# Optimization experiments

Hardware: AMD Instinct MI355X
Metric: run time of the kernel (lower is better)

Reference implementation:

```python
import jax, jax.numpy as jnp
import numpy as np

N = 100000      # nodes
E = 1600000     # edges (avg degree 16)
F_DIM = 64      # input feature
H = 64          # hidden1
D1 = 64         # decoder1
P = 200000      # number of query pairs
EPS = 0.0       # GIN eps (train_eps=False)


def setup_inputs() -> dict:
    key = jax.random.key(0)
    ks = jax.random.split(key, 12)
    x = jax.random.normal(ks[0], (N, F_DIM), jnp.float32)
    edge_index = jax.random.randint(ks[1], (2, E), 0, N, dtype=jnp.int32)
    curvature = jax.random.normal(ks[2], (E,), jnp.float32)
    idx = jax.random.randint(ks[3], (2, P), 0, N, dtype=jnp.int32)
    s1 = 1.0 / np.sqrt(F_DIM)
    s2 = 1.0 / np.sqrt(H)
    s3 = 1.0 / np.sqrt(4 * H)
    s4 = 1.0 / np.sqrt(D1)
    w1 = jax.random.uniform(ks[4], (F_DIM, H), jnp.float32, -s1, s1)
    b1 = jax.random.uniform(ks[5], (H,), jnp.float32, -s1, s1)
    w2 = jax.random.uniform(ks[6], (H, H), jnp.float32, -s2, s2)
    b2 = jax.random.uniform(ks[7], (H,), jnp.float32, -s2, s2)
    dw1 = jax.random.uniform(ks[8], (4 * H, D1), jnp.float32, -s3, s3)
    db1 = jax.random.uniform(ks[9], (D1,), jnp.float32, -s3, s3)
    dw2 = jax.random.uniform(ks[10], (D1, 1), jnp.float32, -s4, s4)
    db2 = jax.random.uniform(ks[11], (1,), jnp.float32, -s4, s4)
    return {"x": x, "edge_index": edge_index, "curvature": curvature, "idx": idx,
            "w1": w1, "b1": b1, "w2": w2, "b2": b2,
            "dw1": dw1, "db1": db1, "dw2": dw2, "db2": db2}


def reference(x, edge_index, curvature, idx, w1, b1, w2, b2, dw1, db1, dw2, db2):
    # curvature path: abs + dropout (eval mode => identity), result unused by output
    _ = jnp.abs(curvature)
    src, dst = edge_index[0], edge_index[1]
    # GIN aggregation with self-loops of weight 1: sum_j x_j + x_i
    agg = jax.ops.segment_sum(x[src], dst, num_segments=N) + x  # [N, F]
    h = (1.0 + EPS) * x + agg
    # nn = Linear -> ReLU -> Linear
    h = jnp.maximum(h @ w1 + b1, 0.0) @ w2 + b2                 # [N, H]
    h = jnp.maximum(h, 0.0)                                     # outer ReLU
    e1 = h[idx[0]]                                              # [P, H]
    e2 = h[idx[1]]                                              # [P, H]
    feat = jnp.concatenate([e1 + e2, e1 * e2, e1, e2], axis=1)  # [P, 4H]
    log = jnp.maximum(feat @ dw1 + db1, 0.0) @ dw2 + db2        # [P, 1]
    return log
```

## Files before the change

kernel.cpp:

```cpp
#include <hip/hip_runtime.h>
#include <hip/hip_bf16.h>
#include <hip/hip_fp16.h>
#include <cstdint>

#define N_NODES 100000
#define N_EDGES 1600000
#define FDIM 64
#define NPAIRS 200000
#define NB 391
#define BCAP 4864
#define SSTR 5632
#define EPB 6250

typedef __attribute__((ext_vector_type(8))) _Float16 half8;
typedef __attribute__((ext_vector_type(4))) float floatx4;

__global__ void __launch_bounds__(256) k0_fused(const float4* __restrict__ x4,
        __half* __restrict__ xh, const int* __restrict__ dst,
        int* __restrict__ matrix, int* __restrict__ ovfCnt) {
    __shared__ int hist[NB];
    int blk = blockIdx.x, tid = threadIdx.x;
    int i = blk * 256 + tid;
    if (i == 0) ovfCnt[0] = 0;
    float4 v = x4[i];
    ushort4 o;
    o.x = __half_as_ushort(__float2half(v.x));
    o.y = __half_as_ushort(__float2half(v.y));
    o.z = __half_as_ushort(__float2half(v.z));
    o.w = __half_as_ushort(__float2half(v.w));
    ((ushort4*)xh)[i] = o;
    if (blk < 256) {
        for (int j = tid; j < NB; j += 256) hist[j] = 0;
        __syncthreads();
        int base = blk * EPB;
        for (int j = tid; j < EPB; j += 256)
            atomicAdd(&hist[dst[base + j] >> 8], 1);
        __syncthreads();
        for (int j = tid; j < NB; j += 256) matrix[blk * NB + j] = hist[j];
    }
}

__global__ void __launch_bounds__(256) p1b_scan(int* __restrict__ matrix,
                                                int* __restrict__ bucketCnt) {
    __shared__ int s[256];
    int b = blockIdx.x, t = threadIdx.x;
    int v = matrix[t * NB + b];
    s[t] = v;
    __syncthreads();
    for (int off = 1; off < 256; off <<= 1) {
        int u = (t >= off) ? s[t - off] : 0;
        __syncthreads();
        s[t] += u;
        __syncthreads();
    }
    matrix[t * NB + b] = s[t] - v;
    if (t == 255) bucketCnt[b] = s[255];
}

__global__ void __launch_bounds__(1024) p1c_scatter(const int* __restrict__ src,
        const int* __restrict__ dst, const int* __restrict__ matrix,
        int* __restrict__ bucketArr, int* __restrict__ ovfCnt,
        int2* __restrict__ ovfList) {
    __shared__ int cur[NB];
    int tid = threadIdx.x, blk = blockIdx.x;
    for (int i = tid; i < NB; i += 1024) cur[i] = matrix[blk * NB + i];
    __syncthreads();
    int base = blk * EPB;
    for (int i = tid; i < EPB; i += 1024) {
        int e = base + i;
        int s = src[e], d = dst[e];
        int b = d >> 8;
        int pos = atomicAdd(&cur[b], 1);
        if (pos < BCAP) {
            bucketArr[(size_t)b * SSTR + pos] = ((d & 255) << 17) | s;
        } else {
            int idx = atomicAdd(ovfCnt, 1);
            ovfList[idx] = make_int2(d, s);
        }
    }
}

__global__ void __launch_bounds__(256) p2_build(int* __restrict__ bucketArr,
        const int* __restrict__ bucketCnt, int* __restrict__ rowptr,
        int* __restrict__ deg) {
    __shared__ int ebuf[BCAP];
    __shared__ int hist[256], sc[256], cur[256];
    int b = blockIdx.x, t = threadIdx.x;
    int cnt = bucketCnt[b];
    if (cnt > BCAP) cnt = BCAP;
    int* arr = bucketArr + (size_t)b * SSTR;
    hist[t] = 0;
    __syncthreads();
    for (int i = t; i < cnt; i += 256) {
        int e = arr[i];
        ebuf[i] = e;
        atomicAdd(&hist[(e >> 17) & 255], 1);
    }
    __syncthreads();
    int h = hist[t];
    int pc = (h + 3) & ~3;
    sc[t] = pc;
    __syncthreads();
    for (int off = 1; off < 256; off <<= 1) {
        int u = (t >= off) ? sc[t - off] : 0;
        __syncthreads();
        sc[t] += u;
        __syncthreads();
    }
    int rbase = sc[t] - pc;
    cur[t] = rbase;
    int n = (b << 8) + t;
    if (n < N_NODES) {
        rowptr[n] = b * SSTR + rbase;
        deg[n] = h;
    }
    __syncthreads();
    for (int i = t; i < cnt; i += 256) {
        int e = ebuf[i];
        int dl = (e >> 17) & 255;
        int pos = atomicAdd(&cur[dl], 1);
        arr[pos] = e & 0x1FFFF;
    }
}

__device__ __forceinline__ void addrow(float4& acc, const __half* __restrict__ xh,
                                       int s, int fq) {
    float2 raw = *(const float2*)(xh + (size_t)s * 64 + fq * 4);
    __half2 a = *(__half2*)&raw.x;
    __half2 b = *(__half2*)&raw.y;
    float2 fa = __half22float2(a);
    float2 fb = __half22float2(b);
    acc.x += fa.x; acc.y += fa.y; acc.z += fb.x; acc.w += fb.y;
}

__global__ void __launch_bounds__(256) k2_agg(const __half* __restrict__ xh,
                       __half* __restrict__ h0h, const int* __restrict__ deg,
                       const int* __restrict__ rowptr, const int* __restrict__ csr,
                       const int* __restrict__ ovfCnt,
                       const int2* __restrict__ ovfList,
                       const float* __restrict__ x) {
    int gid = blockIdx.x * 256 + threadIdx.x;
    int n = gid >> 4, fq = gid & 15;
    int dc = deg[n];
    const int4* srow = (const int4*)(csr + rowptr[n]);
    float2 raw = *(const float2*)(xh + (size_t)n * 64 + fq * 4);
    __half2 sa = *(__half2*)&raw.x;
    __half2 sb = *(__half2*)&raw.y;
    float2 fa = __half22float2(sa);
    float2 fb = __half22float2(sb);
    float4 acc = {2.f * fa.x, 2.f * fa.y, 2.f * fb.x, 2.f * fb.y};
    int oc = ovfCnt[0];
    if (oc > 0) {
        for (int i = 0; i < oc; ++i) {
            int2 e = ovfList[i];
            if (e.x == n) {
                const float* xr = x + (size_t)e.y * 64 + fq * 4;
                acc.x += xr[0]; acc.y += xr[1]; acc.z += xr[2]; acc.w += xr[3];
            }
        }
    }
    for (int i = 0; i < dc; i += 16) {
        int4 s4 = srow[i >> 2];
        int4 s5, s6, s7;
        if (i + 4 < dc)  s5 = srow[(i >> 2) + 1];
        if (i + 8 < dc)  s6 = srow[(i >> 2) + 2];
        if (i + 12 < dc) s7 = srow[(i >> 2) + 3];
        addrow(acc, xh, s4.x, fq);
        if (i + 1 < dc)  addrow(acc, xh, s4.y, fq);
        if (i + 2 < dc)  addrow(acc, xh, s4.z, fq);
        if (i + 3 < dc)  addrow(acc, xh, s4.w, fq);
        if (i + 4 < dc)  addrow(acc, xh, s5.x, fq);
        if (i + 5 < dc)  addrow(acc, xh, s5.y, fq);
        if (i + 6 < dc)  addrow(acc, xh, s5.z, fq);
        if (i + 7 < dc)  addrow(acc, xh, s5.w, fq);
        if (i + 8 < dc)  addrow(acc, xh, s6.x, fq);
        if (i + 9 < dc)  addrow(acc, xh, s6.y, fq);
        if (i + 10 < dc) addrow(acc, xh, s6.z, fq);
        if (i + 11 < dc) addrow(acc, xh, s6.w, fq);
        if (i + 12 < dc) addrow(acc, xh, s7.x, fq);
        if (i + 13 < dc) addrow(acc, xh, s7.y, fq);
        if (i + 14 < dc) addrow(acc, xh, s7.z, fq);
        if (i + 15 < dc) addrow(acc, xh, s7.w, fq);
    }
    ushort4 st;
    st.x = __half_as_ushort(__float2half(acc.x));
    st.y = __half_as_ushort(__float2half(acc.y));
    st.z = __half_as_ushort(__float2half(acc.z));
    st.w = __half_as_ushort(__float2half(acc.w));
    ((ushort4*)h0h)[(size_t)n * 16 + fq] = st;
}

__global__ void __launch_bounds__(256) k3_mfma(const __half* __restrict__ h,
        __half* __restrict__ hh, const float* __restrict__ w1,
        const float* __restrict__ b1, const float* __restrict__ w2,
        const float* __restrict__ b2) {
    __shared__ half8 WF1[512], WF2[512];
    __shared__ float Tbuf[4 * 16 * 68];
    int tid = threadIdx.x;
    for (int f = tid; f < 512; f += 256) {
        int lane = f & 63, st = f >> 6;
        int t = st & 3, kh = st >> 2;
        int q = lane >> 4, nl = lane & 15;
        int n = t * 16 + nl;
        int K0 = kh * 32 + q * 8;
        half8 hv1, hv2;
#pragma unroll
        for (int j = 0; j < 8; ++j) {
            hv1[j] = (_Float16)w1[(K0 + j) * 64 + n];
            hv2[j] = (_Float16)w2[(K0 + j) * 64 + n];
        }
        WF1[f] = hv1;
        WF2[f] = hv2;
    }
    __syncthreads();
    int lane = tid & 63;
    int q = lane >> 4, p = lane & 15;
    int wtid0 = blockIdx.x * 4 + (tid >> 6);
    int wtid = wtid0 < 6249 ? wtid0 : 6249;
    int n0 = wtid * 16;
    float b1t[4], b2t[4];
#pragma unroll
    for (int t = 0; t < 4; ++t) {
        b1t[t] = b1[t * 16 + p];
        b2t[t] = b2[t * 16 + p];
    }
    const half8* hrow = (const half8*)(h + (size_t)(n0 + p) * 64);
    half8 A0 = hrow[q], A1 = hrow[4 + q];
    floatx4 acc[4];
#pragma unroll
    for (int t = 0; t < 4; ++t) acc[t] = (floatx4){0.f, 0.f, 0.f, 0.f};
#pragma unroll
    for (int t = 0; t < 4; ++t) {
        acc[t] = __builtin_amdgcn_mfma_f32_16x16x32_f16(A0, WF1[t * 64 + lane],
                                                        acc[t], 0, 0, 0);
        acc[t] = __builtin_amdgcn_mfma_f32_16x16x32_f16(A1, WF1[(4 + t) * 64 + lane],
                                                        acc[t], 0, 0, 0);
    }
    float* T = Tbuf + (tid >> 6) * (16 * 68);
#pragma unroll
    for (int t = 0; t < 4; ++t) {
#pragma unroll
        for (int r = 0; r < 4; ++r)
            T[(q * 4 + r) * 68 + t * 16 + p] = fmaxf(acc[t][r] + b1t[t], 0.f);
    }
    const float* Tp = T + p * 68;
    float4 u0 = *(const float4*)(Tp + q * 8);
    float4 u1 = *(const float4*)(Tp + q * 8 + 4);
    float4 u2 = *(const float4*)(Tp + 32 + q * 8);
    float4 u3 = *(const float4*)(Tp + 32 + q * 8 + 4);
    half8 g0, g1;
    g0[0] = (_Float16)u0.x; g0[1] = (_Float16)u0.y;
    g0[2] = (_Float16)u0.z; g0[3] = (_Float16)u0.w;
    g0[4] = (_Float16)u1.x; g0[5] = (_Float16)u1.y;
    g0[6] = (_Float16)u1.z; g0[7] = (_Float16)u1.w;
    g1[0] = (_Float16)u2.x; g1[1] = (_Float16)u2.y;
    g1[2] = (_Float16)u2.z; g1[3] = (_Float16)u2.w;
    g1[4] = (_Float16)u3.x; g1[5] = (_Float16)u3.y;
    g1[6] = (_Float16)u3.z; g1[7] = (_Float16)u3.w;
#pragma unroll
    for (int t = 0; t < 4; ++t) acc[t] = (floatx4){0.f, 0.f, 0.f, 0.f};
#pragma unroll
    for (int t = 0; t < 4; ++t) {
        acc[t] = __builtin_amdgcn_mfma_f32_16x16x32_f16(g0, WF2[t * 64 + lane],
                                                        acc[t], 0, 0, 0);
        acc[t] = __builtin_amdgcn_mfma_f32_16x16x32_f16(g1, WF2[(4 + t) * 64 + lane],
                                                        acc[t], 0, 0, 0);
    }
    if (wtid0 < 6250) {
#pragma unroll
        for (int t = 0; t < 4; ++t) {
#pragma unroll
            for (int r = 0; r < 4; ++r)
                hh[(size_t)(n0 + q * 4 + r) * 64 + t * 16 + p] =
                    __float2half(fmaxf(acc[t][r] + b2t[t], 0.f));
        }
    }
}

__global__ void __launch_bounds__(512) k4_pair(const __half* __restrict__ hh,
                        const int* __restrict__ qidx,
                        const float* __restrict__ dw1, const float* __restrict__ db1,
                        const float* __restrict__ dw2, const float* __restrict__ db2,
                        float* __restrict__ out, int numWaves) {
    __shared__ half8 BF[2048];
    int tid = threadIdx.x;
    for (int f = tid; f < 2048; f += 512) {
        int lane = f & 63, st = f >> 6;
        int t = st & 3, s = st >> 2;
        int q = lane >> 4, nl = lane & 15;
        int n = t * 16 + nl;
        int K0 = s * 32 + q * 8;
        half8 hv;
#pragma unroll
        for (int j = 0; j < 8; ++j) hv[j] = (_Float16)dw1[(K0 + j) * 64 + n];
        BF[f] = hv;
    }
    __syncthreads();
    int lane = tid & 63;
    int q = lane >> 4, nl = lane & 15;
    float db1t[4], dw2t[4];
#pragma unroll
    for (int t = 0; t < 4; ++t) {
        db1t[t] = db1[t * 16 + nl];
        dw2t[t] = dw2[t * 16 + nl];
    }
    float db2v = db2[0];
    int wid = (blockIdx.x * 512 + tid) >> 6;
    for (int task = wid; task < NPAIRS / 16; task += numWaves) {
        int p0 = task * 16;
        int i1 = qidx[p0 + nl];
        int i2 = qidx[NPAIRS + p0 + nl];
        const half8* r1 = (const half8*)(hh + (size_t)i1 * 64);
        const half8* r2 = (const half8*)(hh + (size_t)i2 * 64);
        half8 e1a = r1[q],     e1b = r1[4 + q];
        half8 e2a = r2[q],     e2b = r2[4 + q];
        half8 sA = e1a + e2a,  sB = e1b + e2b;
        half8 pA = e1a * e2a,  pB = e1b * e2b;
        floatx4 acc[4];
#pragma unroll
        for (int t = 0; t < 4; ++t) acc[t] = (floatx4){0.f, 0.f, 0.f, 0.f};

#define DO_STEP(S, AV)                                                        \
        _Pragma("unroll")                                                     \
        for (int t = 0; t < 4; ++t)                                           \
            acc[t] = __builtin_amdgcn_mfma_f32_16x16x32_f16(                  \
                (AV), BF[((S) * 4 + t) * 64 + lane], acc[t], 0, 0, 0);

        DO_STEP(0, sA)
        DO_STEP(1, sB)
        DO_STEP(2, pA)
        DO_STEP(3, pB)
        DO_STEP(4, e1a)
        DO_STEP(5, e1b)
        DO_STEP(6, e2a)
        DO_STEP(7, e2b)
#undef DO_STEP

        float part[4] = {0.f, 0.f, 0.f, 0.f};
#pragma unroll
        for (int t = 0; t < 4; ++t) {
#pragma unroll
            for (int r = 0; r < 4; ++r)
                part[r] = fmaf(fmaxf(acc[t][r] + db1t[t], 0.f), dw2t[t], part[r]);
        }
#pragma unroll
        for (int off = 1; off < 16; off <<= 1) {
#pragma unroll
            for (int r = 0; r < 4; ++r) part[r] += __shfl_xor(part[r], off, 64);
        }
        if (nl == 0) {
#pragma unroll
            for (int r = 0; r < 4; ++r) out[p0 + q * 4 + r] = part[r] + db2v;
        }
    }
}

extern "C" void kernel_launch(void* const* d_in, const int* in_sizes, int n_in,
                              void* d_out, int out_size, void* d_ws, size_t ws_size,
                              hipStream_t stream) {
    const float* x    = (const float*)d_in[0];
    const int*   eidx = (const int*)d_in[1];
    const int*   qidx = (const int*)d_in[3];
    const float* w1   = (const float*)d_in[4];
    const float* b1   = (const float*)d_in[5];
    const float* w2   = (const float*)d_in[6];
    const float* b2   = (const float*)d_in[7];
    const float* dw1  = (const float*)d_in[8];
    const float* db1  = (const float*)d_in[9];
    const float* dw2  = (const float*)d_in[10];
    const float* db2  = (const float*)d_in[11];
    float* out = (float*)d_out;

    char* ws = (char*)d_ws;
    __half* h0h       = (__half*)ws;
    __half* xh        = (__half*)(ws + 12800000);
    int*    bucketArr = (int*)(ws + 25600000);
    int2*   ovfList   = (int2*)(ws + 34408448);
    int*    rowptr    = (int*)(ws + 47208448);
    int*    deg       = (int*)(ws + 47608448);
    int*    matrix    = (int*)(ws + 48008448);
    int*    bucketCnt = (int*)(ws + 48408832);
    int*    ovfCnt    = (int*)(ws + 48410396);

    const int* src = eidx;
    const int* dst = eidx + N_EDGES;

    k0_fused<<<6250, 256, 0, stream>>>((const float4*)x, xh, dst, matrix, ovfCnt);
    p1b_scan<<<NB, 256, 0, stream>>>(matrix, bucketCnt);
    p1c_scatter<<<256, 1024, 0, stream>>>(src, dst, matrix, bucketArr,
                                          ovfCnt, ovfList);
    p2_build<<<NB, 256, 0, stream>>>(bucketArr, bucketCnt, rowptr, deg);
    k2_agg<<<6250, 256, 0, stream>>>(xh, h0h, deg, rowptr, bucketArr,
                                     ovfCnt, ovfList, x);
    k3_mfma<<<1563, 256, 0, stream>>>(h0h, xh, w1, b1, w2, b2);
    const int blocks4 = 625;
    k4_pair<<<blocks4, 512, 0, stream>>>(xh, qidx, dw1, db1, dw2, db2, out,
                                         blocks4 * 8);
}
```

Before: 209.4 us.

## Fuse aggregation with node MLP, replace bucket scan with atomics, fold decoder weights

Result: slower. 219.4 us (+4.7%).

```diff
diff --git a/kernel.cpp b/kernel.cpp
--- a/kernel.cpp
+++ b/kernel.cpp
@@ -15,13 +15,13 @@
 typedef __attribute__((ext_vector_type(8))) _Float16 half8;
 typedef __attribute__((ext_vector_type(4))) float floatx4;
 
-__global__ void __launch_bounds__(256) k0_fused(const float4* __restrict__ x4,
-        __half* __restrict__ xh, const int* __restrict__ dst,
-        int* __restrict__ matrix, int* __restrict__ ovfCnt) {
-    __shared__ int hist[NB];
+__global__ void __launch_bounds__(256) k0_prep(const float4* __restrict__ x4,
+        __half* __restrict__ xh, const float* __restrict__ w1,
+        const float* __restrict__ w2, __half* __restrict__ WF1g,
+        __half* __restrict__ WF2g, int* __restrict__ bucketCur,
+        int* __restrict__ ovfCnt) {
     int blk = blockIdx.x, tid = threadIdx.x;
     int i = blk * 256 + tid;
-    if (i == 0) ovfCnt[0] = 0;
     float4 v = x4[i];
     ushort4 o;
     o.x = __half_as_ushort(__float2half(v.x));
@@ -29,43 +29,42 @@
     o.z = __half_as_ushort(__float2half(v.z));
     o.w = __half_as_ushort(__float2half(v.w));
     ((ushort4*)xh)[i] = o;
-    if (blk < 256) {
-        for (int j = tid; j < NB; j += 256) hist[j] = 0;
-        __syncthreads();
-        int base = blk * EPB;
-        for (int j = tid; j < EPB; j += 256)
-            atomicAdd(&hist[dst[base + j] >> 8], 1);
-        __syncthreads();
-        for (int j = tid; j < NB; j += 256) matrix[blk * NB + j] = hist[j];
-    }
-}
-
-__global__ void __launch_bounds__(256) p1b_scan(int* __restrict__ matrix,
-                                                int* __restrict__ bucketCnt) {
-    __shared__ int s[256];
-    int b = blockIdx.x, t = threadIdx.x;
-    int v = matrix[t * NB + b];
-    s[t] = v;
-    __syncthreads();
-    for (int off = 1; off < 256; off <<= 1) {
-        int u = (t >= off) ? s[t - off] : 0;
-        __syncthreads();
-        s[t] += u;
-        __syncthreads();
-    }
-    matrix[t * NB + b] = s[t] - v;
-    if (t == 255) bucketCnt[b] = s[255];
+    if (blk == 0) {
+        for (int j = tid; j < NB; j += 256) bucketCur[j] = 0;
+        if (tid == 0) ovfCnt[0] = 0;
+    } else if (blk <= 2) {
+        const float* w = (blk == 1) ? w1 : w2;
+        __half* dw = (blk == 1) ? WF1g : WF2g;
+        for (int f = tid; f < 512; f += 256) {
+            int lane = f & 63, st = f >> 6;
+            int t = st & 3, kh = st >> 2;
+            int q = lane >> 4, nl = lane & 15;
+            int n = t * 16 + nl;
+            int K0 = kh * 32 + q * 8;
+            half8 hv;
+#pragma unroll
+            for (int j = 0; j < 8; ++j) hv[j] = (_Float16)w[(K0 + j) * 64 + n];
+            ((half8*)dw)[f] = hv;
+        }
+    }
 }
 
 __global__ void __launch_bounds__(1024) p1c_scatter(const int* __restrict__ src,
-        const int* __restrict__ dst, const int* __restrict__ matrix,
-        int* __restrict__ bucketArr, int* __restrict__ ovfCnt,
+        const int* __restrict__ dst, int* __restrict__ bucketArr,
+        int* __restrict__ bucketCur, int* __restrict__ ovfCnt,
         int2* __restrict__ ovfList) {
+    __shared__ int hist[NB];
     __shared__ int cur[NB];
     int tid = threadIdx.x, blk = blockIdx.x;
-    for (int i = tid; i < NB; i += 1024) cur[i] = matrix[blk * NB + i];
+    for (int i = tid; i < NB; i += 1024) hist[i] = 0;
     __syncthreads();
     int base = blk * EPB;
+    for (int i = tid; i < EPB; i += 1024)
+        atomicAdd(&hist[dst[base + i] >> 8], 1);
+    __syncthreads();
+    for (int b = tid; b < NB; b += 1024)
+        cur[b] = atomicAdd(&bucketCur[b], hist[b]);
+    __syncthreads();
     for (int i = tid; i < EPB; i += 1024) {
         int e = base + i;
         int s = src[e], d = dst[e];
@@ -133,14 +132,26 @@
     acc.x += fa.x; acc.y += fa.y; acc.z += fb.x; acc.w += fb.y;
 }
 
-__global__ void __launch_bounds__(256) k2_agg(const __half* __restrict__ xh,
-                       __half* __restrict__ h0h, const int* __restrict__ deg,
-                       const int* __restrict__ rowptr, const int* __restrict__ csr,
-                       const int* __restrict__ ovfCnt,
-                       const int2* __restrict__ ovfList,
-                       const float* __restrict__ x) {
-    int gid = blockIdx.x * 256 + threadIdx.x;
+__global__ void __launch_bounds__(256) k23_agg_mlp(const __half* __restrict__ xh,
+        __half* __restrict__ hh, const int* __restrict__ deg,
+        const int* __restrict__ rowptr, const int* __restrict__ csr,
+        const int* __restrict__ ovfCnt, const int2* __restrict__ ovfList,
+        const float* __restrict__ x, const __half* __restrict__ WF1g,
+        const __half* __restrict__ WF2g, const float* __restrict__ b1,
+        const float* __restrict__ b2) {
+    __shared__ __half h0s[16][72];
+    __shared__ float T[16][68];
+    int tid = threadIdx.x;
+    int gid = blockIdx.x * 256 + tid;
     int n = gid >> 4, fq = gid & 15;
+    int lane = tid & 63, w = tid >> 6;
+    int q = lane >> 4, p = lane & 15;
+    const half8* W1v = (const half8*)WF1g;
+    const half8* W2v = (const half8*)WF2g;
+    half8 wf1a = W1v[w * 64 + lane], wf1b = W1v[(4 + w) * 64 + lane];
+    half8 wf2a = W2v[w * 64 + lane], wf2b = W2v[(4 + w) * 64 + lane];
+    float b1v = b1[w * 16 + p], b2v = b2[w * 16 + p];
+
     int dc = deg[n];
     const int4* srow = (const int4*)(csr + rowptr[n]);
     float2 raw = *(const float2*)(xh + (size_t)n * 64 + fq * 4);
@@ -182,72 +193,27 @@
         if (i + 14 < dc) addrow(acc, xh, s7.z, fq);
         if (i + 15 < dc) addrow(acc, xh, s7.w, fq);
     }
-    ushort4 st;
-    st.x = __half_as_ushort(__float2half(acc.x));
-    st.y = __half_as_ushort(__float2half(acc.y));
-    st.z = __half_as_ushort(__float2half(acc.z));
-    st.w = __half_as_ushort(__float2half(acc.w));
-    ((ushort4*)h0h)[(size_t)n * 16 + fq] = st;
-}
-
-__global__ void __launch_bounds__(256) k3_mfma(const __half* __restrict__ h,
-        __half* __restrict__ hh, const float* __restrict__ w1,
-        const float* __restrict__ b1, const float* __restrict__ w2,
-        const float* __restrict__ b2) {
-    __shared__ half8 WF1[512], WF2[512];
-    __shared__ float Tbuf[4 * 16 * 68];
-    int tid = threadIdx.x;
-    for (int f = tid; f < 512; f += 256) {
-        int lane = f & 63, st = f >> 6;
-        int t = st & 3, kh = st >> 2;
-        int q = lane >> 4, nl = lane & 15;
-        int n = t * 16 + nl;
-        int K0 = kh * 32 + q * 8;
-        half8 hv1, hv2;
-#pragma unroll
-        for (int j = 0; j < 8; ++j) {
-            hv1[j] = (_Float16)w1[(K0 + j) * 64 + n];
-            hv2[j] = (_Float16)w2[(K0 + j) * 64 + n];
-        }
-        WF1[f] = hv1;
-        WF2[f] = hv2;
-    }
-    __syncthreads();
-    int lane = tid & 63;
-    int q = lane >> 4, p = lane & 15;
-    int wtid0 = blockIdx.x * 4 + (tid >> 6);
-    int wtid = wtid0 < 6249 ? wtid0 : 6249;
-    int n0 = wtid * 16;
-    float b1t[4], b2t[4];
-#pragma unroll
-    for (int t = 0; t < 4; ++t) {
-        b1t[t] = b1[t * 16 + p];
-        b2t[t] = b2[t * 16 + p];
-    }
-    const half8* hrow = (const half8*)(h + (size_t)(n0 + p) * 64);
-    half8 A0 = hrow[q], A1 = hrow[4 + q];
-    floatx4 acc[4];
-#pragma unroll
-    for (int t = 0; t < 4; ++t) acc[t] = (floatx4){0.f, 0.f, 0.f, 0.f};
-#pragma unroll
-    for (int t = 0; t < 4; ++t) {
-        acc[t] = __builtin_amdgcn_mfma_f32_16x16x32_f16(A0, WF1[t * 64 + lane],
-                                                        acc[t], 0, 0, 0);
-        acc[t] = __builtin_amdgcn_mfma_f32_16x16x32_f16(A1, WF1[(4 + t) * 64 + lane],
-                                                        acc[t], 0, 0, 0);
-    }
-    float* T = Tbuf + (tid >> 6) * (16 * 68);
-#pragma unroll
-    for (int t = 0; t < 4; ++t) {
-#pragma unroll
-        for (int r = 0; r < 4; ++r)
-            T[(q * 4 + r) * 68 + t * 16 + p] = fmaxf(acc[t][r] + b1t[t], 0.f);
-    }
-    const float* Tp = T + p * 68;
-    float4 u0 = *(const float4*)(Tp + q * 8);
-    float4 u1 = *(const float4*)(Tp + q * 8 + 4);
-    float4 u2 = *(const float4*)(Tp + 32 + q * 8);
-    float4 u3 = *(const float4*)(Tp + 32 + q * 8 + 4);
+    ushort4 st4;
+    st4.x = __half_as_ushort(__float2half(acc.x));
+    st4.y = __half_as_ushort(__float2half(acc.y));
+    st4.z = __half_as_ushort(__float2half(acc.z));
+    st4.w = __half_as_ushort(__float2half(acc.w));
+    *(ushort4*)&h0s[n & 15][fq * 4] = st4;
+    __syncthreads();
+
+    half8 A0 = *(const half8*)&h0s[p][q * 8];
+    half8 A1 = *(const half8*)&h0s[p][32 + q * 8];
+    floatx4 acc1 = (floatx4){0.f, 0.f, 0.f, 0.f};
+    acc1 = __builtin_amdgcn_mfma_f32_16x16x32_f16(A0, wf1a, acc1, 0, 0, 0);
+    acc1 = __builtin_amdgcn_mfma_f32_16x16x32_f16(A1, wf1b, acc1, 0, 0, 0);
+#pragma unroll
+    for (int r = 0; r < 4; ++r)
+        T[q * 4 + r][w * 16 + p] = fmaxf(acc1[r] + b1v, 0.f);
+    __syncthreads();
+    float4 u0 = *(const float4*)&T[p][q * 8];
+    float4 u1 = *(const float4*)&T[p][q * 8 + 4];
+    float4 u2 = *(const float4*)&T[p][32 + q * 8];
+    float4 u3 = *(const float4*)&T[p][32 + q * 8 + 4];
     half8 g0, g1;
     g0[0] = (_Float16)u0.x; g0[1] = (_Float16)u0.y;
     g0[2] = (_Float16)u0.z; g0[3] = (_Float16)u0.w;
@@ -257,24 +223,14 @@
     g1[2] = (_Float16)u2.z; g1[3] = (_Float16)u2.w;
     g1[4] = (_Float16)u3.x; g1[5] = (_Float16)u3.y;
     g1[6] = (_Float16)u3.z; g1[7] = (_Float16)u3.w;
-#pragma unroll
-    for (int t = 0; t < 4; ++t) acc[t] = (floatx4){0.f, 0.f, 0.f, 0.f};
-#pragma unroll
-    for (int t = 0; t < 4; ++t) {
-        acc[t] = __builtin_amdgcn_mfma_f32_16x16x32_f16(g0, WF2[t * 64 + lane],
-                                                        acc[t], 0, 0, 0);
-        acc[t] = __builtin_amdgcn_mfma_f32_16x16x32_f16(g1, WF2[(4 + t) * 64 + lane],
-                                                        acc[t], 0, 0, 0);
-    }
-    if (wtid0 < 6250) {
-#pragma unroll
-        for (int t = 0; t < 4; ++t) {
-#pragma unroll
-            for (int r = 0; r < 4; ++r)
-                hh[(size_t)(n0 + q * 4 + r) * 64 + t * 16 + p] =
-                    __float2half(fmaxf(acc[t][r] + b2t[t], 0.f));
-        }
-    }
+    floatx4 acc2 = (floatx4){0.f, 0.f, 0.f, 0.f};
+    acc2 = __builtin_amdgcn_mfma_f32_16x16x32_f16(g0, wf2a, acc2, 0, 0, 0);
+    acc2 = __builtin_amdgcn_mfma_f32_16x16x32_f16(g1, wf2b, acc2, 0, 0, 0);
+    int n0 = blockIdx.x << 4;
+#pragma unroll
+    for (int r = 0; r < 4; ++r)
+        hh[(size_t)(n0 + q * 4 + r) * 64 + w * 16 + p] =
+            __float2half(fmaxf(acc2[r] + b2v, 0.f));
 }
 
 __global__ void __launch_bounds__(512) k4_pair(const __half* __restrict__ hh,
@@ -282,17 +238,25 @@
                         const float* __restrict__ dw1, const float* __restrict__ db1,
                         const float* __restrict__ dw2, const float* __restrict__ db2,
                         float* __restrict__ out, int numWaves) {
-    __shared__ half8 BF[2048];
+    __shared__ half8 BF[1536];
     int tid = threadIdx.x;
-    for (int f = tid; f < 2048; f += 512) {
+    for (int f = tid; f < 1536; f += 512) {
         int lane = f & 63, st = f >> 6;
         int t = st & 3, s = st >> 2;
+        int sec = s >> 1, kh = s & 1;
         int q = lane >> 4, nl = lane & 15;
         int n = t * 16 + nl;
-        int K0 = s * 32 + q * 8;
+        int K0 = kh * 32 + q * 8;
         half8 hv;
 #pragma unroll
-        for (int j = 0; j < 8; ++j) hv[j] = (_Float16)dw1[(K0 + j) * 64 + n];
+        for (int j = 0; j < 8; ++j) {
+            int k = K0 + j;
+            float v;
+            if (sec == 0)      v = dw1[k * 64 + n] + dw1[(128 + k) * 64 + n];
+            else if (sec == 1) v = dw1[k * 64 + n] + dw1[(192 + k) * 64 + n];
+            else               v = dw1[(64 + k) * 64 + n];
+            hv[j] = (_Float16)v;
+        }
         BF[f] = hv;
     }
     __syncthreads();
@@ -314,7 +278,6 @@
         const half8* r2 = (const half8*)(hh + (size_t)i2 * 64);
         half8 e1a = r1[q],     e1b = r1[4 + q];
         half8 e2a = r2[q],     e2b = r2[4 + q];
-        half8 sA = e1a + e2a,  sB = e1b + e2b;
         half8 pA = e1a * e2a,  pB = e1b * e2b;
         floatx4 acc[4];
 #pragma unroll
@@ -326,14 +289,12 @@
             acc[t] = __builtin_amdgcn_mfma_f32_16x16x32_f16(                  \
                 (AV), BF[((S) * 4 + t) * 64 + lane], acc[t], 0, 0, 0);
 
-        DO_STEP(0, sA)
-        DO_STEP(1, sB)
-        DO_STEP(2, pA)
-        DO_STEP(3, pB)
-        DO_STEP(4, e1a)
-        DO_STEP(5, e1b)
-        DO_STEP(6, e2a)
-        DO_STEP(7, e2b)
+        DO_STEP(0, e1a)
+        DO_STEP(1, e1b)
+        DO_STEP(2, e2a)
+        DO_STEP(3, e2b)
+        DO_STEP(4, pA)
+        DO_STEP(5, pB)
 #undef DO_STEP
 
         float part[4] = {0.f, 0.f, 0.f, 0.f};
@@ -372,28 +333,26 @@
     float* out = (float*)d_out;
 
     char* ws = (char*)d_ws;
-    __half* h0h       = (__half*)ws;
+    __half* hh        = (__half*)ws;
     __half* xh        = (__half*)(ws + 12800000);
     int*    bucketArr = (int*)(ws + 25600000);
     int2*   ovfList   = (int2*)(ws + 34408448);
     int*    rowptr    = (int*)(ws + 47208448);
     int*    deg       = (int*)(ws + 47608448);
-    int*    matrix    = (int*)(ws + 48008448);
-    int*    bucketCnt = (int*)(ws + 48408832);
+    __half* WF1g      = (__half*)(ws + 48008448);
+    __half* WF2g      = (__half*)(ws + 48016640);
+    int*    bucketCur = (int*)(ws + 48408832);
     int*    ovfCnt    = (int*)(ws + 48410396);
 
     const int* src = eidx;
     const int* dst = eidx + N_EDGES;
 
-    k0_fused<<<6250, 256, 0, stream>>>((const float4*)x, xh, dst, matrix, ovfCnt);
-    p1b_scan<<<NB, 256, 0, stream>>>(matrix, bucketCnt);
-    p1c_scatter<<<256, 1024, 0, stream>>>(src, dst, matrix, bucketArr,
+    k0_prep<<<6250, 256, 0, stream>>>((const float4*)x, xh, w1, w2,
+                                      WF1g, WF2g, bucketCur, ovfCnt);
+    p1c_scatter<<<256, 1024, 0, stream>>>(src, dst, bucketArr, bucketCur,
                                           ovfCnt, ovfList);
-    p2_build<<<NB, 256, 0, stream>>>(bucketArr, bucketCnt, rowptr, deg);
-    k2_agg<<<6250, 256, 0, stream>>>(xh, h0h, deg, rowptr, bucketArr,
-                                     ovfCnt, ovfList, x);
-    k3_mfma<<<1563, 256, 0, stream>>>(h0h, xh, w1, b1, w2, b2);
-    const int blocks4 = 625;
-    k4_pair<<<blocks4, 512, 0, stream>>>(xh, qidx, dw1, db1, dw2, db2, out,
-                                         blocks4 * 8);
-}
+    p2_build<<<NB, 256, 0, stream>>>(bucketArr, bucketCur, rowptr, deg);
+    k23_agg_mlp<<<6250, 256, 0, stream>>>(xh, hh, deg, rowptr, bucketArr,
+                                          ovfCnt, ovfList, x, WF1g, WF2g, b1, b2);
+    k4_pair<<<782, 512, 0, stream>>>(hh, qidx, dw1, db1, dw2, db2, out, 6256);
+}
```
